# Performance work log

Measured on AMD Instinct MI355X. Metric: run time of the kernel, lower is better.

## Reference

```python
import jax, jax.numpy as jnp
import numpy as np


def _dwconv(x, w, pad, dil=1):
    # x: [B,C,H,W], w: [C,1,kh,kw] depthwise
    C = x.shape[1]
    return jax.lax.conv_general_dilated(
        x, w, window_strides=(1, 1), padding=[(pad, pad), (pad, pad)],
        rhs_dilation=(dil, dil),
        dimension_numbers=('NCHW', 'OIHW', 'NCHW'),
        feature_group_count=C)


def _conv1x1(x, w, b):
    # w: [O,C,1,1]
    return jnp.einsum('bchw,oc->bohw', x, w[:, :, 0, 0]) + b[None, :, None, None]


def _ln(x, g, b, eps=1e-6):
    mu = x.mean(-1, keepdims=True)
    var = ((x - mu) ** 2).mean(-1, keepdims=True)
    return (x - mu) * jax.lax.rsqrt(var + eps) * g + b


def _gelu(x):
    return jax.nn.gelu(x, approximate=False)  # torch nn.GELU default = exact erf


def _starts(h, step, ps):
    s = []
    for i in range(0, h + step - ps, step):
        s.append(i if i + ps <= h else h - ps)
    return np.asarray(s, np.int32)


def _divisor(h, w, step, ps):
    # replicates patch_reverse's overlap /2 strips exactly
    div = np.ones((h, w), np.float32)
    for i in range(step, h + step - ps, step):
        top, down = i, i + ps - step
        if top + ps > h:
            top = h - ps
        div[top:down, :] *= 2.0
    for j in range(step, w + step - ps, step):
        left, right = j, j + ps - step
        if left + ps > w:
            left = w - ps
        div[:, left:right] *= 2.0
    return div


def _forward(x, ps, lth_dw_w, lth_pw_w, lth_pw_b, lth_gate_w, lth_gate_b, lth_scale,
             ln1_g, ln1_b, ln2_g, ln2_b, qkv_w, gate_w, gate_b, proj_w, pe_w, pe_b,
             fc1_w, fc1_b, dw_w, dw_b, fc2_w, fc2_b):
    B, C, H, W = x.shape
    step = ps - 2
    # ---- Low_to_high ----
    low = x.reshape(B, C, H // 2, 2, W // 2, 2).mean(axis=(3, 5))  # adaptive avg pool (even H,W)
    low_up = jax.image.resize(low, (B, C, H, W), method='bilinear')  # align_corners=False
    hf = x - low_up
    sgate = jax.nn.sigmoid(_conv1x1(jnp.abs(hf), lth_gate_w, lth_gate_b))  # [B,1,H,W]
    refined = _conv1x1(_gelu(_dwconv(hf, lth_dw_w, pad=2, dil=2)), lth_pw_w, lth_pw_b)
    x = x + lth_scale * refined * sgate
    # ---- patch_divide (overlapping windows) ----
    st = ps if (H == ps and W == ps) else step
    tops, lefts = _starts(H, st, ps), _starts(W, st, ps)
    nh, nw = len(tops), len(lefts)
    r = tops[:, None] + np.arange(ps)   # [nh, ps]
    c = lefts[:, None] + np.arange(ps)  # [nw, ps]
    crop = x[:, :, r[:, None, :, None], c[None, :, None, :]]  # [B,C,nh,nw,ps,ps]
    t = crop.transpose(0, 2, 3, 4, 5, 1).reshape(B * nh * nw, ps * ps, C)  # (b n) (h w) c
    # ---- Attention (single-head, qk_dim == dim) ----
    y = _ln(t, ln1_g, ln1_b)
    qkv = y @ qkv_w                      # [Bn, N, 3C]
    q, k, v = jnp.split(qkv, 3, axis=-1)
    z = _gelu(y @ gate_w + gate_b)       # gate
    qimg = q.transpose(0, 2, 1).reshape(-1, C, ps, ps)
    pe = (_dwconv(qimg, pe_w, pad=1) + pe_b[None, :, None, None])
    pe = pe.reshape(-1, C, ps * ps).transpose(0, 2, 1)
    scale = C ** (-0.5)                  # qk_dim = dim = C
    attn = jax.nn.softmax(jnp.einsum('bnc,bmc->bnm', q, k) * scale, axis=-1)
    out = jnp.einsum('bnm,bmc->bnc', attn, v) + pe
    t = (out * z) @ proj_w + t           # proj + residual
    # ---- patch_reverse (overlap-add, strips averaged) ----
    crop = t.reshape(B, nh, nw, ps, ps, C).transpose(0, 5, 1, 2, 3, 4)  # [B,C,nh,nw,ps,ps]
    summed = jnp.zeros_like(x).at[:, :, r[:, None, :, None], c[None, :, None, :]].add(crop)
    x = summed * (1.0 / jnp.asarray(_divisor(H, W, st, ps)))
    # ---- ConvFFN ----
    xt = x.reshape(B, C, H * W).transpose(0, 2, 1)  # [B,HW,C]
    y = _ln(xt, ln2_g, ln2_b)
    y = _gelu(y @ fc1_w + fc1_b)                    # [B,HW,2C]
    yimg = y.transpose(0, 2, 1).reshape(B, -1, H, W)
    y = y + (_dwconv(yimg, dw_w, pad=2) + dw_b[None, :, None, None]).reshape(B, -1, H * W).transpose(0, 2, 1)
    y = y @ fc2_w + fc2_b
    xt = y + xt
    return xt.transpose(0, 2, 1).reshape(B, C, H, W)


def setup_inputs() -> dict:
    key = jax.random.key(0)
    ks = jax.random.split(key, 16)
    B, C, H, W = 8, 128, 128, 128
    HID = 2 * C
    def w(i, shape, s=0.02):
        return jax.random.normal(ks[i], shape, jnp.float32) * s
    return {
        'x': jax.random.normal(ks[0], (B, C, H, W), jnp.float32),
        'ps': 16,
        'lth_dw_w': w(1, (C, 1, 3, 3), 0.1),
        'lth_pw_w': w(2, (C, C, 1, 1)),
        'lth_pw_b': jnp.zeros((C,), jnp.float32),
        'lth_gate_w': w(3, (1, C, 1, 1), 0.1),
        'lth_gate_b': jnp.zeros((1,), jnp.float32),
        'lth_scale': w(4, (1, C, 1, 1), 0.1),
        'ln1_g': jnp.ones((C,), jnp.float32),
        'ln1_b': jnp.zeros((C,), jnp.float32),
        'ln2_g': jnp.ones((C,), jnp.float32),
        'ln2_b': jnp.zeros((C,), jnp.float32),
        'qkv_w': w(5, (C, 3 * C)),
        'gate_w': w(6, (C, C)),
        'gate_b': jnp.zeros((C,), jnp.float32),
        'proj_w': w(7, (C, C)),
        'pe_w': w(8, (C, 1, 3, 3), 0.1),
        'pe_b': jnp.zeros((C,), jnp.float32),
        'fc1_w': w(9, (C, HID)),
        'fc1_b': jnp.zeros((HID,), jnp.float32),
        'dw_w': w(10, (HID, 1, 5, 5), 0.1),
        'dw_b': jnp.zeros((HID,), jnp.float32),
        'fc2_w': w(11, (HID, C)),
        'fc2_b': jnp.zeros((C,), jnp.float32),
    }


def reference(x, ps, lth_dw_w, lth_pw_w, lth_pw_b, lth_gate_w, lth_gate_b, lth_scale,
              ln1_g, ln1_b, ln2_g, ln2_b, qkv_w, gate_w, gate_b, proj_w, pe_w, pe_b,
              fc1_w, fc1_b, dw_w, dw_b, fc2_w, fc2_b):
    return _forward(x, ps, lth_dw_w, lth_pw_w, lth_pw_b, lth_gate_w, lth_gate_b, lth_scale,
                    ln1_g, ln1_b, ln2_g, ln2_b, qkv_w, gate_w, gate_b, proj_w, pe_w, pe_b,
                    fc1_w, fc1_b, dw_w, dw_b, fc2_w, fc2_b)
```

## Files before the change

### kernel.cpp

```cpp
#include <hip/hip_runtime.h>
#include <hip/hip_bf16.h>
#include <math.h>

typedef __hip_bfloat16 bf16;
typedef __attribute__((ext_vector_type(8))) short bf16x8;
typedef __attribute__((ext_vector_type(4))) float f32x4;

static constexpr int B_ = 8, C_ = 128, H_ = 128, W_ = 128;
static constexpr int N_ = H_ * W_;
static constexpr int NWIN = 648;

__device__ __forceinline__ float b2f(bf16 v) { return __bfloat162float(v); }
__device__ __forceinline__ bf16 f2b(float v) { return __float2bfloat16(v); }

__device__ __forceinline__ float gelu_f(float x) {
    float xs = x * 0.70710678118654752f;
    float ax = fabsf(xs);
    float t = 1.0f / fmaf(0.3275911f, ax, 1.0f);
    float poly = t * fmaf(t, fmaf(t, fmaf(t, fmaf(t, 1.061405429f, -1.453152027f), 1.421413741f), -0.284496736f), 0.254829592f);
    float erf_ax = fmaf(-poly, __expf(-ax * ax), 1.0f);
    float erfv = copysignf(erf_ax, xs);
    return 0.5f * x * (1.0f + erfv);
}

__global__ __launch_bounds__(256) void k_wprep(const float* __restrict__ projw, const float* __restrict__ qkvw,
                                               const float* __restrict__ gatew, const float* __restrict__ w1,
                                               const float* __restrict__ w2, const float* __restrict__ pww,
                                               bf16* __restrict__ wt, bf16* __restrict__ wqkv,
                                               bf16* __restrict__ wt1, bf16* __restrict__ wt2,
                                               bf16* __restrict__ wpw) {
    int idx = blockIdx.x * 256 + threadIdx.x;
    if (idx < 16384) {
        int o = idx >> 7, c = idx & 127;
        wt[idx] = f2b(projw[c * 128 + o]);
    } else if (idx < 81920) {
        int i = idx - 16384; int o = i >> 7, c = i & 127;
        wqkv[i] = f2b((o < 384) ? qkvw[c * 384 + o] : gatew[c * 128 + (o - 384)]);
    } else if (idx < 114688) {
        int i = idx - 81920; int o = i >> 7, c = i & 127;
        wt1[i] = f2b(w1[c * 256 + o]);
    } else if (idx < 147456) {
        int i = idx - 114688; int o = i >> 8, c = i & 255;
        wt2[i] = f2b(w2[c * 128 + o]);
    } else {
        int i = idx - 147456;
        wpw[i] = f2b(pww[i]);
    }
}

__global__ __launch_bounds__(256) void k_hf2(const float* __restrict__ x, bf16* __restrict__ hf) {
    __shared__ float lowt[10][64];
    int tid = threadIdx.x;
    int bid = blockIdx.x;
    int ht = bid & 7, c = (bid >> 3) & 127, b = bid >> 10;
    const float* xp = x + (size_t)(b * C_ + c) * N_;
    int h0 = ht * 16;
    int lo0 = (h0 >> 1) - 1;
    for (int e = tid; e < 640; e += 256) {
        int lr = e >> 6, jc = e & 63;
        int j = lo0 + lr; j = j < 0 ? 0 : (j > 63 ? 63 : j);
        const float* pr = xp + (2 * j) * W_ + 2 * jc;
        lowt[lr][jc] = (pr[0] + pr[1] + pr[W_] + pr[W_ + 1]) * 0.25f;
    }
    __syncthreads();
    int hl = tid >> 4, wg = tid & 15;
    int h = h0 + hl;
    int jh = h >> 1;
    int j0, j1; float wh0, wh1;
    if (h & 1) { j0 = jh; j1 = jh + 1 > 63 ? 63 : jh + 1; wh0 = 0.75f; wh1 = 0.25f; }
    else       { j0 = jh - 1 < 0 ? 0 : jh - 1; j1 = jh;   wh0 = 0.25f; wh1 = 0.75f; }
    int l0 = j0 - lo0, l1 = j1 - lo0;
    float4 xa = *(const float4*)(xp + h * W_ + wg * 8);
    float4 xb = *(const float4*)(xp + h * W_ + wg * 8 + 4);
    float xv[8] = {xa.x, xa.y, xa.z, xa.w, xb.x, xb.y, xb.z, xb.w};
    union { bf16 hh[8]; uint4 u; } outv;
    #pragma unroll
    for (int k2 = 0; k2 < 8; ++k2) {
        int w = wg * 8 + k2;
        int jw = w >> 1;
        int w0, w1; float ww0, ww1;
        if (w & 1) { w0 = jw; w1 = jw + 1 > 63 ? 63 : jw + 1; ww0 = 0.75f; ww1 = 0.25f; }
        else       { w0 = jw - 1 < 0 ? 0 : jw - 1; w1 = jw;   ww0 = 0.25f; ww1 = 0.75f; }
        float up = wh0 * (ww0 * lowt[l0][w0] + ww1 * lowt[l0][w1])
                 + wh1 * (ww0 * lowt[l1][w0] + ww1 * lowt[l1][w1]);
        outv.hh[k2] = f2b(xv[k2] - up);
    }
    *(uint4*)(hf + (size_t)(b * C_ + c) * N_ + h * W_ + wg * 8) = outv.u;
}

__global__ __launch_bounds__(256) void k_sgate(const bf16* __restrict__ hf, const float* __restrict__ gw,
                                               const float* __restrict__ gb, float* __restrict__ sg) {
    int idx = blockIdx.x * 256 + threadIdx.x;
    int n = idx & (N_ - 1); int b = idx >> 14;
    const bf16* p = hf + (size_t)b * C_ * N_ + n;
    float s = 0.f;
    for (int c = 0; c < C_; ++c) s += gw[c] * fabsf(b2f(p[(size_t)c * N_]));
    s += gb[0];
    sg[idx] = 1.0f / (1.0f + __expf(-s));
}

__global__ __launch_bounds__(256) void k_dw3t(const bf16* __restrict__ hf, const float* __restrict__ wdw,
                                              bf16* __restrict__ g) {
    __shared__ __align__(16) char tile[5760];
    int tid = threadIdx.x;
    int bid = blockIdx.x;
    int ht = bid & 7, ch = (bid >> 3) & 127, b = bid >> 10;
    const bf16* p = hf + (size_t)(b * C_ + ch) * N_;
    for (int e = tid; e < 360; e += 256) *(uint4*)(tile + e * 16) = (uint4){0, 0, 0, 0};
    __syncthreads();
    int h0 = ht * 16 - 2;
    for (int e = tid; e < 320; e += 256) {
        int lr = e >> 4, slot = e & 15;
        int gr = h0 + lr;
        if ((unsigned)gr < 128u) {
            uint4 val = *(const uint4*)(p + gr * 128 + slot * 8);
            *(uint4*)(tile + lr * 288 + 16 + slot * 16) = val;
        }
    }
    float kw[9];
    #pragma unroll
    for (int j = 0; j < 9; ++j) kw[j] = wdw[ch * 9 + j];
    __syncthreads();
    int hl = tid >> 4, wg = tid & 15, w = wg * 8;
    float acc[8] = {};
    #pragma unroll
    for (int ky = 0; ky < 3; ++ky) {
        int base = (hl + 2 * ky) * 288 + 2 * w;
        union { uint4 u; bf16 h[8]; } c0, c1, c2;
        c0.u = *(const uint4*)(tile + base);
        c1.u = *(const uint4*)(tile + base + 16);
        c2.u = *(const uint4*)(tile + base + 32);
        float e[12];
        e[0] = b2f(c0.h[6]); e[1] = b2f(c0.h[7]);
        #pragma unroll
        for (int j = 0; j < 8; ++j) e[2 + j] = b2f(c1.h[j]);
        e[10] = b2f(c2.h[0]); e[11] = b2f(c2.h[1]);
        #pragma unroll
        for (int ow = 0; ow < 8; ++ow) {
            acc[ow] = fmaf(kw[ky * 3 + 0], e[ow], acc[ow]);
            acc[ow] = fmaf(kw[ky * 3 + 1], e[ow + 2], acc[ow]);
            acc[ow] = fmaf(kw[ky * 3 + 2], e[ow + 4], acc[ow]);
        }
    }
    union { bf16 h[8]; uint4 u; } outv;
    #pragma unroll
    for (int ow = 0; ow < 8; ++ow) outv.h[ow] = f2b(gelu_f(acc[ow]));
    *(uint4*)(g + (size_t)(b * C_ + ch) * N_ + (ht * 16 + hl) * 128 + w) = outv.u;
}

__global__ __launch_bounds__(256) void k_pw_mfma(const bf16* __restrict__ g, const bf16* __restrict__ wpw,
                                                 const float* __restrict__ pwb, const float* __restrict__ x,
                                                 const float* __restrict__ scale, const float* __restrict__ sg,
                                                 bf16* __restrict__ x1) {
    __shared__ __align__(16) char lds[49152];
    int tid = threadIdx.x;
    int lane = tid & 63, w = tid >> 6;
    int l15 = lane & 15, lhi = lane >> 4;
    int gtok = blockIdx.x * 64; int b = gtok >> 14; int nb = gtok & (N_ - 1);
    char* wch = lds + 16384;
    for (int e = tid; e < 8192; e += 256) {
        int c = e >> 6, i = e & 63;
        bf16 val = g[(size_t)(b * C_ + c) * N_ + nb + i];
        *(bf16*)(lds + i * 256 + ((2 * c) ^ ((i & 7) << 4))) = val;
    }
    for (int e = tid; e < 2048; e += 256) {
        int row = e >> 4, slot = e & 15;
        uint4 val = *(const uint4*)((const char*)wpw + row * 256 + slot * 16);
        *(uint4*)(wch + row * 256 + ((slot * 16) ^ ((row & 7) << 4))) = val;
    }
    __syncthreads();
    bf16x8 afr[4];
    {
        int row = w * 16 + l15;
        #pragma unroll
        for (int cc = 0; cc < 4; ++cc) {
            int cbyt = cc * 64 + lhi * 16;
            afr[cc] = *(const bf16x8*)(lds + row * 256 + (cbyt ^ ((row & 7) << 4)));
        }
    }
    f32x4 acc[8];
    #pragma unroll
    for (int t = 0; t < 8; ++t) acc[t] = (f32x4){0.f, 0.f, 0.f, 0.f};
    #pragma unroll
    for (int ot = 0; ot < 8; ++ot) {
        int row = ot * 16 + l15;
        #pragma unroll
        for (int cc = 0; cc < 4; ++cc) {
            int cbyt = cc * 64 + lhi * 16;
            bf16x8 bfr = *(const bf16x8*)(wch + row * 256 + (cbyt ^ ((row & 7) << 4)));
            acc[ot] = __builtin_amdgcn_mfma_f32_16x16x32_bf16(afr[cc], bfr, acc[ot], 0, 0, 0);
        }
    }
    int n0 = nb + w * 16 + lhi * 4;
    float4 sg4 = *(const float4*)&sg[b * N_ + n0];
    #pragma unroll
    for (int ot = 0; ot < 8; ++ot) {
        int o = ot * 16 + l15;
        size_t obase = (size_t)(b * C_ + o) * N_ + n0;
        float4 x4 = *(const float4*)&x[obase];
        float sc = scale[o], bi = pwb[o];
        union { bf16 h[4]; uint2 u; } t4;
        t4.h[0] = f2b(x4.x + sc * (acc[ot][0] + bi) * sg4.x);
        t4.h[1] = f2b(x4.y + sc * (acc[ot][1] + bi) * sg4.y);
        t4.h[2] = f2b(x4.z + sc * (acc[ot][2] + bi) * sg4.z);
        t4.h[3] = f2b(x4.w + sc * (acc[ot][3] + bi) * sg4.w);
        *(uint2*)(x1 + obase) = t4.u;
    }
}

__global__ __launch_bounds__(256) void k_qkv_mfma(const bf16* __restrict__ x1, const float* __restrict__ lng,
                                                  const float* __restrict__ lnb, const bf16* __restrict__ wall,
                                                  const float* __restrict__ gateb,
                                                  bf16* __restrict__ q, bf16* __restrict__ k,
                                                  bf16* __restrict__ v, bf16* __restrict__ z) {
    __shared__ __align__(16) char lds[49664];
    __shared__ float red2[8][64];
    __shared__ float mu_l[64], rs_l[64];
    int tid = threadIdx.x;
    int lane = tid & 63, w = tid >> 6;
    int l15 = lane & 15, lhi = lane >> 4;
    int win = blockIdx.x >> 2; int qbase = (blockIdx.x & 3) * 64;
    int b = win / 81; int r0 = win % 81; int top = (r0 / 9) * 14, left = (r0 % 9) * 14;
    float* xf = (float*)(lds + 16384);
    char* wchunk = lds + 16384;
    for (int e = tid; e < 8192; e += 256) {
        int c = e >> 6, i = e & 63; int tok = qbase + i; int p = tok >> 4, qq = tok & 15;
        xf[c * 65 + i] = b2f(x1[(size_t)(b * C_ + c) * N_ + (top + p) * W_ + (left + qq)]);
    }
    __syncthreads();
    {
        int i = tid & 63, r = tid >> 6;
        float s = 0.f, ss = 0.f;
        for (int cc = r * 32; cc < r * 32 + 32; ++cc) { float vv = xf[cc * 65 + i]; s += vv; ss += vv * vv; }
        red2[r][i] = s; red2[4 + r][i] = ss;
    }
    __syncthreads();
    if (tid < 64) {
        float s = red2[0][tid] + red2[1][tid] + red2[2][tid] + red2[3][tid];
        float ss = red2[4][tid] + red2[5][tid] + red2[6][tid] + red2[7][tid];
        float mu = s * (1.f / 128.f); float var = ss * (1.f / 128.f) - mu * mu;
        mu_l[tid] = mu; rs_l[tid] = rsqrtf(var + 1e-6f);
    }
    __syncthreads();
    {
        int c = tid & 127;
        float g = lng[c], be = lnb[c];
        for (int e = tid; e < 8192; e += 256) {
            int i = e >> 7;
            float val = (xf[c * 65 + i] - mu_l[i]) * rs_l[i] * g + be;
            *(bf16*)(lds + i * 256 + ((2 * c) ^ ((i & 7) << 4))) = f2b(val);
        }
    }
    __syncthreads();
    bf16x8 afr[4];
    {
        int row = w * 16 + l15;
        #pragma unroll
        for (int cc = 0; cc < 4; ++cc) {
            int cbyt = cc * 64 + lhi * 16;
            afr[cc] = *(const bf16x8*)(lds + row * 256 + (cbyt ^ ((row & 7) << 4)));
        }
    }
    for (int pass = 0; pass < 4; ++pass) {
        __syncthreads();
        for (int e = tid; e < 2048; e += 256) {
            int row = e >> 4, slot = e & 15;
            uint4 val = *(const uint4*)((const char*)wall + (size_t)(pass * 128 + row) * 256 + slot * 16);
            *(uint4*)(wchunk + row * 256 + ((slot * 16) ^ ((row & 7) << 4))) = val;
        }
        __syncthreads();
        f32x4 acc[8];
        #pragma unroll
        for (int t = 0; t < 8; ++t) acc[t] = (f32x4){0.f, 0.f, 0.f, 0.f};
        #pragma unroll
        for (int ot = 0; ot < 8; ++ot) {
            int row = ot * 16 + l15;
            #pragma unroll
            for (int cc = 0; cc < 4; ++cc) {
                int cbyt = cc * 64 + lhi * 16;
                bf16x8 bfr = *(const bf16x8*)(wchunk + row * 256 + (cbyt ^ ((row & 7) << 4)));
                acc[ot] = __builtin_amdgcn_mfma_f32_16x16x32_bf16(afr[cc], bfr, acc[ot], 0, 0, 0);
            }
        }
        if (pass != 2) {
            bf16* outp = (pass == 0) ? q : (pass == 1) ? k : z;
            bool gel = (pass == 3);
            #pragma unroll
            for (int ot = 0; ot < 8; ++ot) {
                int o = ot * 16 + l15;
                float gb = gel ? gateb[o] : 0.f;
                #pragma unroll
                for (int r = 0; r < 4; ++r) {
                    int gtok = qbase + w * 16 + lhi * 4 + r;
                    float vv = acc[ot][r];
                    outp[((size_t)win * 256 + gtok) * 128 + o] = gel ? f2b(gelu_f(vv + gb)) : f2b(vv);
                }
            }
        } else {
            #pragma unroll
            for (int ot = 0; ot < 8; ++ot) {
                int o = ot * 16 + l15;
                union { bf16 h[4]; uint2 u; } t4;
                #pragma unroll
                for (int r = 0; r < 4; ++r) t4.h[r] = f2b(acc[ot][r]);
                *(uint2*)(v + (size_t)win * 32768 + (size_t)o * 256 + qbase + w * 16 + lhi * 4) = t4.u;
            }
        }
    }
}

__global__ __launch_bounds__(256) void k_attn_mfma(const bf16* __restrict__ qb, const bf16* __restrict__ kb,
                                                   const bf16* __restrict__ vb, bf16* __restrict__ ob) {
    __shared__ __align__(16) char lds[49152];
    int tid = threadIdx.x;
    int lane = tid & 63, w = tid >> 6;
    int l15 = lane & 15, lhi = lane >> 4;
    int win = blockIdx.x >> 2, qbase = (blockIdx.x & 3) * 64;
    const bf16* qg = qb + ((size_t)win * 256 + qbase) * 128;
    const bf16* kg = kb + (size_t)win * 256 * 128;
    const bf16* vg = vb + (size_t)win * 128 * 256;
    char* chunk = lds + 32768;
    for (int e = tid; e < 1024; e += 256) {
        int row = e >> 4, slot = e & 15;
        uint4 val = *(const uint4*)((const char*)qg + row * 256 + slot * 16);
        *(uint4*)(lds + row * 256 + ((slot * 16) ^ ((row & 7) << 4))) = val;
    }
    __syncthreads();
    bf16x8 afr[4];
    {
        int row = w * 16 + l15;
        #pragma unroll
        for (int cc = 0; cc < 4; ++cc) {
            int cb = cc * 64 + lhi * 16;
            afr[cc] = *(const bf16x8*)(lds + row * 256 + (cb ^ ((row & 7) << 4)));
        }
    }
    f32x4 acc[16];
    #pragma unroll
    for (int t = 0; t < 16; ++t) acc[t] = (f32x4){0.f, 0.f, 0.f, 0.f};
    for (int kc = 0; kc < 4; ++kc) {
        __syncthreads();
        for (int e = tid; e < 1024; e += 256) {
            int row = e >> 4, slot = e & 15;
            uint4 val = *(const uint4*)((const char*)kg + (size_t)(kc * 64 + row) * 256 + slot * 16);
            *(uint4*)(chunk + row * 256 + ((slot * 16) ^ ((row & 7) << 4))) = val;
        }
        __syncthreads();
        #pragma unroll
        for (int t = 0; t < 4; ++t) {
            int row = t * 16 + l15;
            #pragma unroll
            for (int cc = 0; cc < 4; ++cc) {
                int cb = cc * 64 + lhi * 16;
                bf16x8 bfr = *(const bf16x8*)(chunk + row * 256 + (cb ^ ((row & 7) << 4)));
                acc[kc * 4 + t] = __builtin_amdgcn_mfma_f32_16x16x32_bf16(afr[cc], bfr, acc[kc * 4 + t], 0, 0, 0);
            }
        }
    }
    const float sm_scale = 0.08838834764831845f;
    #pragma unroll
    for (int r = 0; r < 4; ++r) {
        float m = -1e30f;
        #pragma unroll
        for (int t = 0; t < 16; ++t) m = fmaxf(m, acc[t][r]);
        #pragma unroll
        for (int d2 = 1; d2 < 16; d2 <<= 1) m = fmaxf(m, __shfl_xor(m, d2, 64));
        float ssum = 0.f;
        #pragma unroll
        for (int t = 0; t < 16; ++t) { float p = __expf((acc[t][r] - m) * sm_scale); acc[t][r] = p; ssum += p; }
        #pragma unroll
        for (int d2 = 1; d2 < 16; d2 <<= 1) ssum += __shfl_xor(ssum, d2, 64);
        float inv = 1.f / ssum;
        #pragma unroll
        for (int t = 0; t < 16; ++t) acc[t][r] *= inv;
    }
    #pragma unroll
    for (int t = 0; t < 16; ++t) {
        #pragma unroll
        for (int r = 0; r < 4; ++r) {
            int row = w * 16 + lhi * 4 + r;
            int cb = (t * 16 + l15) * 2;
            *(bf16*)(lds + row * 512 + (cb ^ ((row & 7) << 4))) = f2b(acc[t][r]);
        }
    }
    f32x4 oacc[8];
    #pragma unroll
    for (int t = 0; t < 8; ++t) oacc[t] = (f32x4){0.f, 0.f, 0.f, 0.f};
    for (int vc = 0; vc < 4; ++vc) {
        __syncthreads();
        for (int e = tid; e < 1024; e += 256) {
            int row = e >> 3, slot = e & 7;
            uint4 val = *(const uint4*)((const char*)vg + (size_t)row * 512 + vc * 128 + slot * 16);
            *(uint4*)(chunk + row * 128 + ((slot * 16) ^ ((row & 7) << 4))) = val;
        }
        __syncthreads();
        #pragma unroll
        for (int jc = 0; jc < 2; ++jc) {
            int prow = w * 16 + l15;
            int pcb = vc * 128 + jc * 64 + lhi * 16;
            bf16x8 ap = *(const bf16x8*)(lds + prow * 512 + (pcb ^ ((prow & 7) << 4)));
            #pragma unroll
            for (int ct = 0; ct < 8; ++ct) {
                int vrow = ct * 16 + l15;
                int vcb = jc * 64 + lhi * 16;
                bf16x8 bv = *(const bf16x8*)(chunk + vrow * 128 + (vcb ^ ((vrow & 7) << 4)));
                oacc[ct] = __builtin_amdgcn_mfma_f32_16x16x32_bf16(ap, bv, oacc[ct], 0, 0, 0);
            }
        }
    }
    bf16* og = ob + ((size_t)win * 256 + qbase) * 128;
    #pragma unroll
    for (int ct = 0; ct < 8; ++ct) {
        #pragma unroll
        for (int r = 0; r < 4; ++r) {
            int row = w * 16 + lhi * 4 + r;
            og[row * 128 + ct * 16 + l15] = f2b(oacc[ct][r]);
        }
    }
}

__global__ __launch_bounds__(256) void k_peg(bf16* __restrict__ ob, const bf16* __restrict__ qb,
                                             const bf16* __restrict__ zb,
                                             const float* __restrict__ pew, const float* __restrict__ peb) {
    __shared__ float pw_lds[1152];
    __shared__ float pb_lds[128];
    int tid = threadIdx.x;
    for (int e = tid; e < 1152; e += 256) pw_lds[e] = pew[e];
    if (tid < 128) pb_lds[tid] = peb[tid];
    __syncthreads();
    int g = blockIdx.x * 256 + tid;
    int c8 = g & 15, tok = (g >> 4) & 255, win = g >> 12;
    int cb = c8 * 8;
    int pp = tok >> 4, qq = tok & 15;
    size_t base = ((size_t)win * 256 + tok) * 128 + cb;
    float pv[8];
    #pragma unroll
    for (int cc = 0; cc < 8; ++cc) pv[cc] = pb_lds[cb + cc];
    #pragma unroll
    for (int ky = 0; ky < 3; ++ky) {
        int py = pp + ky - 1; if ((unsigned)py >= 16u) continue;
        #pragma unroll
        for (int kx = 0; kx < 3; ++kx) {
            int qx = qq + kx - 1; if ((unsigned)qx >= 16u) continue;
            union { uint4 u; bf16 h[8]; } qu;
            qu.u = *(const uint4*)(qb + ((size_t)win * 256 + py * 16 + qx) * 128 + cb);
            #pragma unroll
            for (int cc = 0; cc < 8; ++cc)
                pv[cc] += pw_lds[(cb + cc) * 9 + ky * 3 + kx] * b2f(qu.h[cc]);
        }
    }
    union { uint4 u; bf16 h[8]; } ou, zu, ru;
    ou.u = *(const uint4*)(ob + base);
    zu.u = *(const uint4*)(zb + base);
    #pragma unroll
    for (int cc = 0; cc < 8; ++cc)
        ru.h[cc] = f2b((b2f(ou.h[cc]) + pv[cc]) * b2f(zu.h[cc]));
    *(uint4*)(ob + base) = ru.u;
}

__global__ __launch_bounds__(256) void k_proj(const bf16* __restrict__ ub, const bf16* __restrict__ wt,
                                              const bf16* __restrict__ x1, bf16* __restrict__ t2) {
    __shared__ __align__(16) char lds[49152];
    int tid = threadIdx.x;
    int lane = tid & 63, w = tid >> 6;
    int l15 = lane & 15, lhi = lane >> 4;
    int win = blockIdx.x >> 2, qbase = (blockIdx.x & 3) * 64;
    int b = win / 81; int r0 = win % 81; int top = (r0 / 9) * 14, left = (r0 % 9) * 14;
    const bf16* ug = ub + ((size_t)win * 256 + qbase) * 128;
    char* wchunk = lds + 16384;
    for (int e = tid; e < 1024; e += 256) {
        int row = e >> 4, slot = e & 15;
        uint4 val = *(const uint4*)((const char*)ug + row * 256 + slot * 16);
        *(uint4*)(lds + row * 256 + ((slot * 16) ^ ((row & 7) << 4))) = val;
    }
    for (int e = tid; e < 2048; e += 256) {
        int row = e >> 4, slot = e & 15;
        uint4 val = *(const uint4*)((const char*)wt + row * 256 + slot * 16);
        *(uint4*)(wchunk + row * 256 + ((slot * 16) ^ ((row & 7) << 4))) = val;
    }
    __syncthreads();
    bf16x8 afr[4];
    {
        int row = w * 16 + l15;
        #pragma unroll
        for (int cc = 0; cc < 4; ++cc) {
            int cbyt = cc * 64 + lhi * 16;
            afr[cc] = *(const bf16x8*)(lds + row * 256 + (cbyt ^ ((row & 7) << 4)));
        }
    }
    f32x4 acc[8];
    #pragma unroll
    for (int t = 0; t < 8; ++t) acc[t] = (f32x4){0.f, 0.f, 0.f, 0.f};
    #pragma unroll
    for (int ot = 0; ot < 8; ++ot) {
        int row = ot * 16 + l15;
        #pragma unroll
        for (int cc = 0; cc < 4; ++cc) {
            int cbyt = cc * 64 + lhi * 16;
            bf16x8 bfr = *(const bf16x8*)(wchunk + row * 256 + (cbyt ^ ((row & 7) << 4)));
            acc[ot] = __builtin_amdgcn_mfma_f32_16x16x32_bf16(afr[cc], bfr, acc[ot], 0, 0, 0);
        }
    }
    #pragma unroll
    for (int ot = 0; ot < 8; ++ot) {
        #pragma unroll
        for (int r = 0; r < 4; ++r) {
            int tok = w * 16 + lhi * 4 + r;
            int o = ot * 16 + l15;
            int gtok = qbase + tok;
            int p = gtok >> 4, qq = gtok & 15;
            float res = b2f(x1[(size_t)(b * C_ + o) * N_ + (top + p) * W_ + (left + qq)]);
            t2[(size_t)win * 32768 + (size_t)o * 256 + gtok] = f2b(acc[ot][r] + res);
        }
    }
}

__global__ __launch_bounds__(256) void k_fold(const bf16* __restrict__ t2, bf16* __restrict__ x2) {
    int idx = blockIdx.x * 256 + threadIdx.x;
    int w = idx & 127, h = (idx >> 7) & 127, c = (idx >> 14) & 127, b = idx >> 21;
    int imin = (h < 16) ? 0 : (h - 2) / 14; int imax = h / 14; if (imax > 8) imax = 8;
    int jmin = (w < 16) ? 0 : (w - 2) / 14; int jmax = w / 14; if (jmax > 8) jmax = 8;
    float sum = 0.f;
    for (int i = imin; i <= imax; ++i)
        for (int j = jmin; j <= jmax; ++j) {
            int win = (b * 9 + i) * 9 + j;
            sum += b2f(t2[(size_t)win * 32768 + c * 256 + (h - i * 14) * 16 + (w - j * 14)]);
        }
    int cnt = (imax - imin + 1) * (jmax - jmin + 1);
    x2[idx] = f2b(sum / (float)cnt);
}

__global__ __launch_bounds__(256) void k_fc1ln(const bf16* __restrict__ x2, const float* __restrict__ lng,
                                               const float* __restrict__ lnb, const bf16* __restrict__ wt1,
                                               const float* __restrict__ b1, bf16* __restrict__ h1) {
    __shared__ __align__(16) char lds[49664];
    __shared__ float red2[8][64];
    __shared__ float mu_l[64], rs_l[64];
    int tid = threadIdx.x;
    int lane = tid & 63, w = tid >> 6;
    int l15 = lane & 15, lhi = lane >> 4;
    int gtok = blockIdx.x * 64; int b = gtok >> 14; int nb = gtok & (N_ - 1);
    float* xf = (float*)(lds + 16384);
    char* wch = lds + 16384;
    for (int e = tid; e < 8192; e += 256) {
        int c = e >> 6, i = e & 63;
        xf[c * 65 + i] = b2f(x2[(size_t)(b * C_ + c) * N_ + nb + i]);
    }
    __syncthreads();
    {
        int i = tid & 63, r = tid >> 6;
        float s = 0.f, ss = 0.f;
        for (int cc = r * 32; cc < r * 32 + 32; ++cc) { float vv = xf[cc * 65 + i]; s += vv; ss += vv * vv; }
        red2[r][i] = s; red2[4 + r][i] = ss;
    }
    __syncthreads();
    if (tid < 64) {
        float s = red2[0][tid] + red2[1][tid] + red2[2][tid] + red2[3][tid];
        float ss = red2[4][tid] + red2[5][tid] + red2[6][tid] + red2[7][tid];
        float mu = s * (1.f / 128.f); float var = ss * (1.f / 128.f) - mu * mu;
        mu_l[tid] = mu; rs_l[tid] = rsqrtf(var + 1e-6f);
    }
    __syncthreads();
    {
        int c = tid & 127;
        float g = lng[c], be = lnb[c];
        for (int e = tid; e < 8192; e += 256) {
            int i = e >> 7;
            float val = (xf[c * 65 + i] - mu_l[i]) * rs_l[i] * g + be;
            *(bf16*)(lds + i * 256 + ((2 * c) ^ ((i & 7) << 4))) = f2b(val);
        }
    }
    __syncthreads();
    bf16x8 afr[4];
    {
        int row = w * 16 + l15;
        #pragma unroll
        for (int cc = 0; cc < 4; ++cc) {
            int cbyt = cc * 64 + lhi * 16;
            afr[cc] = *(const bf16x8*)(lds + row * 256 + (cbyt ^ ((row & 7) << 4)));
        }
    }
    for (int p = 0; p < 2; ++p) {
        __syncthreads();
        for (int e = tid; e < 2048; e += 256) {
            int row = e >> 4, slot = e & 15;
            uint4 val = *(const uint4*)((const char*)wt1 + (size_t)(p * 128 + row) * 256 + slot * 16);
            *(uint4*)(wch + row * 256 + ((slot * 16) ^ ((row & 7) << 4))) = val;
        }
        __syncthreads();
        f32x4 acc[8];
        #pragma unroll
        for (int t = 0; t < 8; ++t) acc[t] = (f32x4){0.f, 0.f, 0.f, 0.f};
        #pragma unroll
        for (int ot = 0; ot < 8; ++ot) {
            int row = ot * 16 + l15;
            #pragma unroll
            for (int cc = 0; cc < 4; ++cc) {
                int cbyt = cc * 64 + lhi * 16;
                bf16x8 bfr = *(const bf16x8*)(wch + row * 256 + (cbyt ^ ((row & 7) << 4)));
                acc[ot] = __builtin_amdgcn_mfma_f32_16x16x32_bf16(afr[cc], bfr, acc[ot], 0, 0, 0);
            }
        }
        int n0 = nb + w * 16 + lhi * 4;
        #pragma unroll
        for (int ot = 0; ot < 8; ++ot) {
            int o = p * 128 + ot * 16 + l15;
            float bi = b1[o];
            union { bf16 h[4]; uint2 u; } t4;
            #pragma unroll
            for (int r = 0; r < 4; ++r) t4.h[r] = f2b(gelu_f(acc[ot][r] + bi));
            *(uint2*)(h1 + (size_t)(b * 256 + o) * N_ + n0) = t4.u;
        }
    }
}

__global__ __launch_bounds__(256) void k_dw5t(const bf16* __restrict__ h1, const float* __restrict__ wdw,
                                              const float* __restrict__ bdw, bf16* __restrict__ h2) {
    __shared__ __align__(16) char tile[5760];
    int tid = threadIdx.x;
    int bid = blockIdx.x;
    int ht = bid & 7, ch = (bid >> 3) & 255, b = bid >> 11;
    const bf16* p = h1 + (size_t)(b * 256 + ch) * N_;
    for (int e = tid; e < 360; e += 256) *(uint4*)(tile + e * 16) = (uint4){0, 0, 0, 0};
    __syncthreads();
    int h0 = ht * 16 - 2;
    for (int e = tid; e < 320; e += 256) {
        int lr = e >> 4, slot = e & 15;
        int gr = h0 + lr;
        if ((unsigned)gr < 128u) {
            uint4 val = *(const uint4*)(p + gr * 128 + slot * 8);
            *(uint4*)(tile + lr * 288 + 16 + slot * 16) = val;
        }
    }
    float kw[25];
    #pragma unroll
    for (int j = 0; j < 25; ++j) kw[j] = wdw[ch * 25 + j];
    float bi = bdw[ch];
    __syncthreads();
    int hl = tid >> 4, wg = tid & 15, w = wg * 8;
    float acc[8];
    #pragma unroll
    for (int ow = 0; ow < 8; ++ow) acc[ow] = bi;
    #pragma unroll
    for (int ky = 0; ky < 5; ++ky) {
        int base = (hl + ky) * 288 + 2 * w;
        union { uint4 u; bf16 h[8]; } c0, c1, c2;
        c0.u = *(const uint4*)(tile + base);
        c1.u = *(const uint4*)(tile + base + 16);
        c2.u = *(const uint4*)(tile + base + 32);
        float e[12];
        e[0] = b2f(c0.h[6]); e[1] = b2f(c0.h[7]);
        #pragma unroll
        for (int j = 0; j < 8; ++j) e[2 + j] = b2f(c1.h[j]);
        e[10] = b2f(c2.h[0]); e[11] = b2f(c2.h[1]);
        #pragma unroll
        for (int ow = 0; ow < 8; ++ow) {
            #pragma unroll
            for (int kx = 0; kx < 5; ++kx)
                acc[ow] = fmaf(kw[ky * 5 + kx], e[ow + kx], acc[ow]);
        }
        if (ky == 2) {
            #pragma unroll
            for (int ow = 0; ow < 8; ++ow) acc[ow] += e[ow + 2];
        }
    }
    union { bf16 h[8]; uint4 u; } outv;
    #pragma unroll
    for (int ow = 0; ow < 8; ++ow) outv.h[ow] = f2b(acc[ow]);
    *(uint4*)(h2 + (size_t)(b * 256 + ch) * N_ + (ht * 16 + hl) * 128 + w) = outv.u;
}

__global__ __launch_bounds__(256) void k_fc2_mfma(const bf16* __restrict__ h2, const bf16* __restrict__ wt2,
                                                  const float* __restrict__ b2, const bf16* __restrict__ x2,
                                                  float* __restrict__ out) {
    __shared__ __align__(16) char lds[65536];
    int tid = threadIdx.x;
    int lane = tid & 63, w = tid >> 6;
    int l15 = lane & 15, lhi = lane >> 4;
    int gtok = blockIdx.x * 64; int b = gtok >> 14; int nb = gtok & (N_ - 1);
    char* wch = lds + 32768;
    for (int e = tid; e < 16384; e += 256) {
        int c = e >> 6, i = e & 63;
        bf16 val = h2[(size_t)(b * 256 + c) * N_ + nb + i];
        *(bf16*)(lds + i * 512 + ((2 * c) ^ ((i & 7) << 4))) = val;
    }
    __syncthreads();
    bf16x8 afr[8];
    {
        int row = w * 16 + l15;
        #pragma unroll
        for (int cc = 0; cc < 8; ++cc) {
            int cbyt = cc * 64 + lhi * 16;
            afr[cc] = *(const bf16x8*)(lds + row * 512 + (cbyt ^ ((row & 7) << 4)));
        }
    }
    f32x4 acc[8];
    #pragma unroll
    for (int t = 0; t < 8; ++t) acc[t] = (f32x4){0.f, 0.f, 0.f, 0.f};
    for (int kh = 0; kh < 2; ++kh) {
        __syncthreads();
        for (int e = tid; e < 2048; e += 256) {
            int row = e >> 4, slot = e & 15;
            uint4 val = *(const uint4*)((const char*)wt2 + (size_t)row * 512 + kh * 256 + slot * 16);
            *(uint4*)(wch + row * 256 + ((slot * 16) ^ ((row & 7) << 4))) = val;
        }
        __syncthreads();
        #pragma unroll
        for (int ot = 0; ot < 8; ++ot) {
            int row = ot * 16 + l15;
            #pragma unroll
            for (int cc = 0; cc < 4; ++cc) {
                int cbyt = cc * 64 + lhi * 16;
                bf16x8 bfr = *(const bf16x8*)(wch + row * 256 + (cbyt ^ ((row & 7) << 4)));
                acc[ot] = __builtin_amdgcn_mfma_f32_16x16x32_bf16(afr[kh * 4 + cc], bfr, acc[ot], 0, 0, 0);
            }
        }
    }
    int n0 = nb + w * 16 + lhi * 4;
    #pragma unroll
    for (int ot = 0; ot < 8; ++ot) {
        int o = ot * 16 + l15;
        size_t obase = (size_t)(b * C_ + o) * N_ + n0;
        float bi = b2[o];
        union { uint2 u; bf16 h[4]; } xr;
        xr.u = *(const uint2*)(x2 + obase);
        float4 r4;
        r4.x = acc[ot][0] + bi + b2f(xr.h[0]);
        r4.y = acc[ot][1] + bi + b2f(xr.h[1]);
        r4.z = acc[ot][2] + bi + b2f(xr.h[2]);
        r4.w = acc[ot][3] + bi + b2f(xr.h[3]);
        *(float4*)(out + obase) = r4;
    }
}

extern "C" void kernel_launch(void* const* d_in, const int* in_sizes, int n_in,
                              void* d_out, int out_size, void* d_ws, size_t ws_size,
                              hipStream_t stream) {
    const float* x         = (const float*)d_in[0];
    const float* lth_dw_w  = (const float*)d_in[2];
    const float* lth_pw_w  = (const float*)d_in[3];
    const float* lth_pw_b  = (const float*)d_in[4];
    const float* lth_gate_w= (const float*)d_in[5];
    const float* lth_gate_b= (const float*)d_in[6];
    const float* lth_scale = (const float*)d_in[7];
    const float* ln1_g     = (const float*)d_in[8];
    const float* ln1_b     = (const float*)d_in[9];
    const float* ln2_g     = (const float*)d_in[10];
    const float* ln2_b     = (const float*)d_in[11];
    const float* qkv_w     = (const float*)d_in[12];
    const float* gate_w    = (const float*)d_in[13];
    const float* gate_b    = (const float*)d_in[14];
    const float* proj_w    = (const float*)d_in[15];
    const float* pe_w      = (const float*)d_in[16];
    const float* pe_b      = (const float*)d_in[17];
    const float* fc1_w     = (const float*)d_in[18];
    const float* fc1_b     = (const float*)d_in[19];
    const float* dw_w      = (const float*)d_in[20];
    const float* dw_b      = (const float*)d_in[21];
    const float* fc2_w     = (const float*)d_in[22];
    const float* fc2_b     = (const float*)d_in[23];

    char* ws = (char*)d_ws;
    constexpr size_t SZ_X = 33554432;
    constexpr size_t SZ_W = 42467328;
    constexpr size_t OFF_A = 0;
    constexpr size_t OFF_B = OFF_A + SZ_X;
    constexpr size_t OFF_C = OFF_B + SZ_W;
    constexpr size_t OFF_D = OFF_C + SZ_W;
    constexpr size_t OFF_E = OFF_D + SZ_W;
    constexpr size_t OFF_F = OFF_E + SZ_W;
    constexpr size_t OFF_G = OFF_F + SZ_W;
    constexpr size_t OFF_H = OFF_G + 32768;
    constexpr size_t OFF_I = OFF_H + 131072;

    bf16*  x1  = (bf16*)(ws + OFF_A);
    bf16*  h2  = (bf16*)(ws + OFF_A);
    float* sg  = (float*)(ws + OFF_B + 16777216);
    bf16*  o   = (bf16*)(ws + OFF_B);
    bf16*  q   = (bf16*)(ws + OFF_C);
    bf16*  x2  = (bf16*)(ws + OFF_C);
    bf16*  hf  = (bf16*)(ws + OFF_D);
    bf16*  k   = (bf16*)(ws + OFF_D);
    bf16*  t2  = (bf16*)(ws + OFF_D);
    bf16*  h1  = (bf16*)(ws + OFF_D);
    bf16*  g   = (bf16*)(ws + OFF_E);
    bf16*  v   = (bf16*)(ws + OFF_E);
    bf16*  z   = (bf16*)(ws + OFF_F);
    bf16*  wt  = (bf16*)(ws + OFF_G);
    bf16*  wqkv= (bf16*)(ws + OFF_H);
    bf16*  wt1 = (bf16*)(ws + OFF_I);
    bf16*  wt2 = (bf16*)(ws + OFF_I + 65536);
    bf16*  wpw = (bf16*)(ws + OFF_I + 131072);

    k_wprep   <<<640,   256, 0, stream>>>(proj_w, qkv_w, gate_w, fc1_w, fc2_w, lth_pw_w,
                                          wt, wqkv, wt1, wt2, wpw);
    k_hf2     <<<8192,  256, 0, stream>>>(x, hf);
    k_sgate   <<<512,   256, 0, stream>>>(hf, lth_gate_w, lth_gate_b, sg);
    k_dw3t    <<<8192,  256, 0, stream>>>(hf, lth_dw_w, g);
    k_pw_mfma <<<2048,  256, 0, stream>>>(g, wpw, lth_pw_b, x, lth_scale, sg, x1);
    k_qkv_mfma<<<2592,  256, 0, stream>>>(x1, ln1_g, ln1_b, wqkv, gate_b, q, k, v, z);
    k_attn_mfma<<<2592, 256, 0, stream>>>(q, k, v, o);
    k_peg     <<<10368, 256, 0, stream>>>(o, q, z, pe_w, pe_b);
    k_proj    <<<2592,  256, 0, stream>>>(o, wt, x1, t2);
    k_fold    <<<65536, 256, 0, stream>>>(t2, x2);
    k_fc1ln   <<<2048,  256, 0, stream>>>(x2, ln2_g, ln2_b, wt1, fc1_b, h1);
    k_dw5t    <<<16384, 256, 0, stream>>>(h1, dw_w, dw_b, h2);
    k_fc2_mfma<<<2048,  256, 0, stream>>>(h2, wt2, fc2_b, x2, (float*)d_out);
}
```

Baseline: 599.8 us.

## Fuse patch fold into fc1+LN kernel and tile depthwise convs per plane

Removes the standalone fold kernel: the fc1+LayerNorm kernel now gathers and averages overlapping window outputs directly from t2, keeps them in LDS, and also writes x2 for the later residual. Both depthwise convolutions now process a whole 128x128 channel plane per block, with each thread computing 8 rows from a sliding register ring of input rows. This removes halo reloads and cuts block count. The cost is larger LDS per block (lower occupancy), more registers, and scattered gather loads inside fc1ln. h1 is moved to a different workspace slot so it does not overwrite t2, which fc1ln still reads.

```diff
diff --git a/kernel.cpp b/kernel.cpp
--- a/kernel.cpp
+++ b/kernel.cpp
@@ -21,6 +21,18 @@
     float erf_ax = fmaf(-poly, __expf(-ax * ax), 1.0f);
     float erfv = copysignf(erf_ax, xs);
     return 0.5f * x * (1.0f + erfv);
+}
+
+__device__ __forceinline__ void load_row12(const char* tile, int a, int wg, float* dst) {
+    int base = a * 288 + wg * 16;
+    union { uint4 u; bf16 hh[8]; } c0, c1, c2;
+    c0.u = *(const uint4*)(tile + base);
+    c1.u = *(const uint4*)(tile + base + 16);
+    c2.u = *(const uint4*)(tile + base + 32);
+    dst[0] = b2f(c0.hh[6]); dst[1] = b2f(c0.hh[7]);
+    #pragma unroll
+    for (int j = 0; j < 8; ++j) dst[2 + j] = b2f(c1.hh[j]);
+    dst[10] = b2f(c2.hh[0]); dst[11] = b2f(c2.hh[1]);
 }
 
 __global__ __launch_bounds__(256) void k_wprep(const float* __restrict__ projw, const float* __restrict__ qkvw,
@@ -99,53 +111,49 @@
     sg[idx] = 1.0f / (1.0f + __expf(-s));
 }
 
-__global__ __launch_bounds__(256) void k_dw3t(const bf16* __restrict__ hf, const float* __restrict__ wdw,
+__global__ __launch_bounds__(256) void k_dw3p(const bf16* __restrict__ hf, const float* __restrict__ wdw,
                                               bf16* __restrict__ g) {
-    __shared__ __align__(16) char tile[5760];
+    __shared__ __align__(16) char tile[38016];
     int tid = threadIdx.x;
     int bid = blockIdx.x;
-    int ht = bid & 7, ch = (bid >> 3) & 127, b = bid >> 10;
+    int ch = bid & 127, b = bid >> 7;
     const bf16* p = hf + (size_t)(b * C_ + ch) * N_;
-    for (int e = tid; e < 360; e += 256) *(uint4*)(tile + e * 16) = (uint4){0, 0, 0, 0};
-    __syncthreads();
-    int h0 = ht * 16 - 2;
-    for (int e = tid; e < 320; e += 256) {
-        int lr = e >> 4, slot = e & 15;
-        int gr = h0 + lr;
-        if ((unsigned)gr < 128u) {
-            uint4 val = *(const uint4*)(p + gr * 128 + slot * 8);
-            *(uint4*)(tile + lr * 288 + 16 + slot * 16) = val;
-        }
+    for (int e = tid; e < 2376; e += 256) *(uint4*)(tile + e * 16) = (uint4){0, 0, 0, 0};
+    __syncthreads();
+    for (int e = tid; e < 2048; e += 256) {
+        int gr = e >> 4, slot = e & 15;
+        uint4 val = *(const uint4*)(p + gr * 128 + slot * 8);
+        *(uint4*)(tile + (gr + 2) * 288 + 16 + slot * 16) = val;
     }
     float kw[9];
     #pragma unroll
     for (int j = 0; j < 9; ++j) kw[j] = wdw[ch * 9 + j];
     __syncthreads();
-    int hl = tid >> 4, wg = tid & 15, w = wg * 8;
-    float acc[8] = {};
-    #pragma unroll
-    for (int ky = 0; ky < 3; ++ky) {
-        int base = (hl + 2 * ky) * 288 + 2 * w;
-        union { uint4 u; bf16 h[8]; } c0, c1, c2;
-        c0.u = *(const uint4*)(tile + base);
-        c1.u = *(const uint4*)(tile + base + 16);
-        c2.u = *(const uint4*)(tile + base + 32);
-        float e[12];
-        e[0] = b2f(c0.h[6]); e[1] = b2f(c0.h[7]);
-        #pragma unroll
-        for (int j = 0; j < 8; ++j) e[2 + j] = b2f(c1.h[j]);
-        e[10] = b2f(c2.h[0]); e[11] = b2f(c2.h[1]);
-        #pragma unroll
-        for (int ow = 0; ow < 8; ++ow) {
-            acc[ow] = fmaf(kw[ky * 3 + 0], e[ow], acc[ow]);
-            acc[ow] = fmaf(kw[ky * 3 + 1], e[ow + 2], acc[ow]);
-            acc[ow] = fmaf(kw[ky * 3 + 2], e[ow + 4], acc[ow]);
-        }
-    }
-    union { bf16 h[8]; uint4 u; } outv;
-    #pragma unroll
-    for (int ow = 0; ow < 8; ++ow) outv.h[ow] = f2b(gelu_f(acc[ow]));
-    *(uint4*)(g + (size_t)(b * C_ + ch) * N_ + (ht * 16 + hl) * 128 + w) = outv.u;
+    int hg = tid >> 4, wg = tid & 15;
+    int h0 = hg * 8;
+    float ring[5][12];
+    #pragma unroll
+    for (int j = 0; j < 4; ++j) load_row12(tile, h0 + j, wg, ring[j]);
+    bf16* op = g + (size_t)(b * C_ + ch) * N_;
+    #pragma unroll
+    for (int rr = 0; rr < 8; ++rr) {
+        load_row12(tile, h0 + rr + 4, wg, ring[(rr + 4) % 5]);
+        float acc[8] = {};
+        #pragma unroll
+        for (int ky = 0; ky < 3; ++ky) {
+            const float* e = ring[(rr + 2 * ky) % 5];
+            #pragma unroll
+            for (int ow = 0; ow < 8; ++ow) {
+                acc[ow] = fmaf(kw[ky * 3 + 0], e[ow], acc[ow]);
+                acc[ow] = fmaf(kw[ky * 3 + 1], e[ow + 2], acc[ow]);
+                acc[ow] = fmaf(kw[ky * 3 + 2], e[ow + 4], acc[ow]);
+            }
+        }
+        union { bf16 h[8]; uint4 u; } outv;
+        #pragma unroll
+        for (int ow = 0; ow < 8; ++ow) outv.h[ow] = f2b(gelu_f(acc[ow]));
+        *(uint4*)(op + (h0 + rr) * 128 + wg * 8) = outv.u;
+    }
 }
 
 __global__ __launch_bounds__(256) void k_pw_mfma(const bf16* __restrict__ g, const bf16* __restrict__ wpw,
@@ -515,24 +523,10 @@
     }
 }
 
-__global__ __launch_bounds__(256) void k_fold(const bf16* __restrict__ t2, bf16* __restrict__ x2) {
-    int idx = blockIdx.x * 256 + threadIdx.x;
-    int w = idx & 127, h = (idx >> 7) & 127, c = (idx >> 14) & 127, b = idx >> 21;
-    int imin = (h < 16) ? 0 : (h - 2) / 14; int imax = h / 14; if (imax > 8) imax = 8;
-    int jmin = (w < 16) ? 0 : (w - 2) / 14; int jmax = w / 14; if (jmax > 8) jmax = 8;
-    float sum = 0.f;
-    for (int i = imin; i <= imax; ++i)
-        for (int j = jmin; j <= jmax; ++j) {
-            int win = (b * 9 + i) * 9 + j;
-            sum += b2f(t2[(size_t)win * 32768 + c * 256 + (h - i * 14) * 16 + (w - j * 14)]);
-        }
-    int cnt = (imax - imin + 1) * (jmax - jmin + 1);
-    x2[idx] = f2b(sum / (float)cnt);
-}
-
-__global__ __launch_bounds__(256) void k_fc1ln(const bf16* __restrict__ x2, const float* __restrict__ lng,
+__global__ __launch_bounds__(256) void k_fc1ln(const bf16* __restrict__ t2, const float* __restrict__ lng,
                                                const float* __restrict__ lnb, const bf16* __restrict__ wt1,
-                                               const float* __restrict__ b1, bf16* __restrict__ h1) {
+                                               const float* __restrict__ b1, bf16* __restrict__ h1,
+                                               bf16* __restrict__ x2w) {
     __shared__ __align__(16) char lds[49664];
     __shared__ float red2[8][64];
     __shared__ float mu_l[64], rs_l[64];
@@ -540,11 +534,24 @@
     int lane = tid & 63, w = tid >> 6;
     int l15 = lane & 15, lhi = lane >> 4;
     int gtok = blockIdx.x * 64; int b = gtok >> 14; int nb = gtok & (N_ - 1);
+    int h = nb >> 7, w0 = nb & 127;
+    int imin = (h < 16) ? 0 : (h - 2) / 14; int imax = h / 14; if (imax > 8) imax = 8;
     float* xf = (float*)(lds + 16384);
     char* wch = lds + 16384;
     for (int e = tid; e < 8192; e += 256) {
         int c = e >> 6, i = e & 63;
-        xf[c * 65 + i] = b2f(x2[(size_t)(b * C_ + c) * N_ + nb + i]);
+        int wp = w0 + i;
+        int jmin = (wp < 16) ? 0 : (wp - 2) / 14; int jmax = wp / 14; if (jmax > 8) jmax = 8;
+        float sum = 0.f;
+        for (int ii = imin; ii <= imax; ++ii)
+            for (int jj = jmin; jj <= jmax; ++jj) {
+                int win = (b * 9 + ii) * 9 + jj;
+                sum += b2f(t2[(size_t)win * 32768 + (size_t)c * 256 + (h - ii * 14) * 16 + (wp - jj * 14)]);
+            }
+        int cnt = (imax - imin + 1) * (jmax - jmin + 1);
+        float val = sum / (float)cnt;
+        xf[c * 65 + i] = val;
+        x2w[(size_t)(b * C_ + c) * N_ + nb + i] = f2b(val);
     }
     __syncthreads();
     {
@@ -614,60 +621,57 @@
     }
 }
 
-__global__ __launch_bounds__(256) void k_dw5t(const bf16* __restrict__ h1, const float* __restrict__ wdw,
+__global__ __launch_bounds__(256) void k_dw5p(const bf16* __restrict__ h1, const float* __restrict__ wdw,
                                               const float* __restrict__ bdw, bf16* __restrict__ h2) {
-    __shared__ __align__(16) char tile[5760];
+    __shared__ __align__(16) char tile[38016];
     int tid = threadIdx.x;
     int bid = blockIdx.x;
-    int ht = bid & 7, ch = (bid >> 3) & 255, b = bid >> 11;
+    int ch = bid & 255, b = bid >> 8;
     const bf16* p = h1 + (size_t)(b * 256 + ch) * N_;
-    for (int e = tid; e < 360; e += 256) *(uint4*)(tile + e * 16) = (uint4){0, 0, 0, 0};
-    __syncthreads();
-    int h0 = ht * 16 - 2;
-    for (int e = tid; e < 320; e += 256) {
-        int lr = e >> 4, slot = e & 15;
-        int gr = h0 + lr;
-        if ((unsigned)gr < 128u) {
-            uint4 val = *(const uint4*)(p + gr * 128 + slot * 8);
-            *(uint4*)(tile + lr * 288 + 16 + slot * 16) = val;
-        }
+    for (int e = tid; e < 2376; e += 256) *(uint4*)(tile + e * 16) = (uint4){0, 0, 0, 0};
+    __syncthreads();
+    for (int e = tid; e < 2048; e += 256) {
+        int gr = e >> 4, slot = e & 15;
+        uint4 val = *(const uint4*)(p + gr * 128 + slot * 8);
+        *(uint4*)(tile + (gr + 2) * 288 + 16 + slot * 16) = val;
     }
     float kw[25];
     #pragma unroll
     for (int j = 0; j < 25; ++j) kw[j] = wdw[ch * 25 + j];
     float bi = bdw[ch];
     __syncthreads();
-    int hl = tid >> 4, wg = tid & 15, w = wg * 8;
-    float acc[8];
-    #pragma unroll
-    for (int ow = 0; ow < 8; ++ow) acc[ow] = bi;
-    #pragma unroll
-    for (int ky = 0; ky < 5; ++ky) {
-        int base = (hl + ky) * 288 + 2 * w;
-        union { uint4 u; bf16 h[8]; } c0, c1, c2;
-        c0.u = *(const uint4*)(tile + base);
-        c1.u = *(const uint4*)(tile + base + 16);
-        c2.u = *(const uint4*)(tile + base + 32);
-        float e[12];
-        e[0] = b2f(c0.h[6]); e[1] = b2f(c0.h[7]);
-        #pragma unroll
-        for (int j = 0; j < 8; ++j) e[2 + j] = b2f(c1.h[j]);
-        e[10] = b2f(c2.h[0]); e[11] = b2f(c2.h[1]);
-        #pragma unroll
-        for (int ow = 0; ow < 8; ++ow) {
-            #pragma unroll
-            for (int kx = 0; kx < 5; ++kx)
-                acc[ow] = fmaf(kw[ky * 5 + kx], e[ow + kx], acc[ow]);
-        }
-        if (ky == 2) {
+    int hg = tid >> 4, wg = tid & 15;
+    int h0 = hg * 8;
+    float ring[5][12];
+    #pragma unroll
+    for (int j = 0; j < 4; ++j) load_row12(tile, h0 + j, wg, ring[j]);
+    bf16* op = h2 + (size_t)(b * 256 + ch) * N_;
+    #pragma unroll
+    for (int rr = 0; rr < 8; ++rr) {
+        load_row12(tile, h0 + rr + 4, wg, ring[(rr + 4) % 5]);
+        float acc[8];
+        #pragma unroll
+        for (int ow = 0; ow < 8; ++ow) acc[ow] = bi;
+        #pragma unroll
+        for (int ky = 0; ky < 5; ++ky) {
+            const float* e = ring[(rr + ky) % 5];
+            #pragma unroll
+            for (int ow = 0; ow < 8; ++ow) {
+                #pragma unroll
+                for (int kx = 0; kx < 5; ++kx)
+                    acc[ow] = fmaf(kw[ky * 5 + kx], e[ow + kx], acc[ow]);
+            }
+        }
+        {
+            const float* e = ring[(rr + 2) % 5];
             #pragma unroll
             for (int ow = 0; ow < 8; ++ow) acc[ow] += e[ow + 2];
         }
-    }
-    union { bf16 h[8]; uint4 u; } outv;
-    #pragma unroll
-    for (int ow = 0; ow < 8; ++ow) outv.h[ow] = f2b(acc[ow]);
-    *(uint4*)(h2 + (size_t)(b * 256 + ch) * N_ + (ht * 16 + hl) * 128 + w) = outv.u;
+        union { bf16 h[8]; uint4 u; } outv;
+        #pragma unroll
+        for (int ow = 0; ow < 8; ++ow) outv.h[ow] = f2b(acc[ow]);
+        *(uint4*)(op + (h0 + rr) * 128 + wg * 8) = outv.u;
+    }
 }
 
 __global__ __launch_bounds__(256) void k_fc2_mfma(const bf16* __restrict__ h2, const bf16* __restrict__ wt2,
@@ -782,9 +786,9 @@
     bf16*  hf  = (bf16*)(ws + OFF_D);
     bf16*  k   = (bf16*)(ws + OFF_D);
     bf16*  t2  = (bf16*)(ws + OFF_D);
-    bf16*  h1  = (bf16*)(ws + OFF_D);
     bf16*  g   = (bf16*)(ws + OFF_E);
     bf16*  v   = (bf16*)(ws + OFF_E);
+    bf16*  h1  = (bf16*)(ws + OFF_E);
     bf16*  z   = (bf16*)(ws + OFF_F);
     bf16*  wt  = (bf16*)(ws + OFF_G);
     bf16*  wqkv= (bf16*)(ws + OFF_H);
@@ -796,14 +800,13 @@
                                           wt, wqkv, wt1, wt2, wpw);
     k_hf2     <<<8192,  256, 0, stream>>>(x, hf);
     k_sgate   <<<512,   256, 0, stream>>>(hf, lth_gate_w, lth_gate_b, sg);
-    k_dw3t    <<<8192,  256, 0, stream>>>(hf, lth_dw_w, g);
+    k_dw3p    <<<1024,  256, 0, stream>>>(hf, lth_dw_w, g);
     k_pw_mfma <<<2048,  256, 0, stream>>>(g, wpw, lth_pw_b, x, lth_scale, sg, x1);
     k_qkv_mfma<<<2592,  256, 0, stream>>>(x1, ln1_g, ln1_b, wqkv, gate_b, q, k, v, z);
     k_attn_mfma<<<2592, 256, 0, stream>>>(q, k, v, o);
     k_peg     <<<10368, 256, 0, stream>>>(o, q, z, pe_w, pe_b);
     k_proj    <<<2592,  256, 0, stream>>>(o, wt, x1, t2);
-    k_fold    <<<65536, 256, 0, stream>>>(t2, x2);
-    k_fc1ln   <<<2048,  256, 0, stream>>>(x2, ln2_g, ln2_b, wt1, fc1_b, h1);
-    k_dw5t    <<<16384, 256, 0, stream>>>(h1, dw_w, dw_b, h2);
+    k_fc1ln   <<<2048,  256, 0, stream>>>(t2, ln2_g, ln2_b, wt1, fc1_b, h1, x2);
+    k_dw5p    <<<2048,  256, 0, stream>>>(h1, dw_w, dw_b, h2);
     k_fc2_mfma<<<2048,  256, 0, stream>>>(h2, wt2, fc2_b, x2, (float*)d_out);
 }
```

Result: faster. 556.3 us (-7.2%).
